# Kernel optimization log

Hardware: AMD Instinct MI355X
Metric: run time of the kernel (lower is better)

The kernel has to match this reference:

```python
import jax, jax.numpy as jnp
import numpy as np

VOCAB, D = 10000, 32
QUEUE_LEN = 100


def setup_inputs() -> dict:
    key = jax.random.key(0)
    ks = jax.random.split(key, 8)
    B, T = 64, 1024
    s = 0.1
    return dict(
        inputs=jax.random.randint(ks[0], (B, T), 0, 10000, dtype=jnp.int32),
        emb=jax.random.normal(ks[1], (VOCAB, D), dtype=jnp.float32) * s,
        k_lstm=jax.random.normal(ks[2], (D, 4 * D), dtype=jnp.float32) * s,
        rk_lstm=jax.random.normal(ks[3], (D, 4 * D), dtype=jnp.float32) * s,
        b_lstm=jnp.zeros((4 * D,), dtype=jnp.float32),
        W1=jax.random.normal(ks[4], (D, D), dtype=jnp.float32) * s,
        b1=jnp.zeros((D,), dtype=jnp.float32),
        W2=jax.random.normal(ks[5], (D, 1), dtype=jnp.float32) * s,
        b2=jnp.zeros((1,), dtype=jnp.float32),
    )


def _lstm(x, k, rk, b):
    # Keras LSTM, gate order [i, f, g(cell), o], sigmoid recurrent act, tanh act.
    B, T, D = x.shape
    xg = jnp.einsum('btd,de->bte', x, k) + b  # precompute input projections

    def step(carry, xg_t):
        h, c = carry
        z = xg_t + h @ rk
        i, f, g, o = jnp.split(z, 4, axis=-1)
        c = jax.nn.sigmoid(f) * c + jax.nn.sigmoid(i) * jnp.tanh(g)
        h = jax.nn.sigmoid(o) * jnp.tanh(c)
        return (h, c), h

    init = (jnp.zeros((B, D), x.dtype), jnp.zeros((B, D), x.dtype))
    _, hs = jax.lax.scan(step, init, jnp.swapaxes(xg, 0, 1))  # [T,B,D]
    return jnp.swapaxes(hs, 0, 1)  # [B,T,D]


def _zero_index_queue(x_ids):
    # Vectorized replacement of the (i,j) Python scan: last QUEUE_LEN positions
    # (row-major order) where token==0, as [QUEUE_LEN,2] int32, padded with -1.
    B, T = x_ids.shape
    flat = (x_ids == 0).reshape(-1)
    N = flat.shape[0]
    ridx = jnp.nonzero(flat[::-1], size=QUEUE_LEN, fill_value=-1)[0]
    pos = jnp.where(ridx >= 0, N - 1 - ridx, -1)[::-1]  # ascending, like deque
    ii = jnp.where(pos >= 0, pos // T, -1)
    jj = jnp.where(pos >= 0, pos % T, -1)
    return jnp.stack([ii, jj], axis=-1).astype(jnp.int32)


def _forward_float(x_ids, emb, k_lstm, rk_lstm, b_lstm, W1, b1, W2, b2):
    x = emb[x_ids]                                  # [B,T,D]
    h = _lstm(x, k_lstm, rk_lstm, b_lstm)           # [B,T,D]
    scores = jnp.einsum('btd,bsd->bts', h, h)       # unscaled dot attention
    attn = jax.nn.softmax(scores, axis=-1)
    ctx = jnp.einsum('bts,bsd->btd', attn, h)       # Keras Attention output
    y = jnp.einsum('btd,bte->bde', ctx, h)          # Dot(axes=(1,1)) -> [B,D,D]
    y = jax.nn.relu(y @ W1 + b1)
    return jax.nn.sigmoid(y @ W2 + b2)              # [B,D,1]


def reference(inputs, emb, k_lstm, rk_lstm, b_lstm, W1, b1, W2, b2):
    x_ids = jnp.where(inputs < VOCAB, inputs, 0)
    out = _forward_float(x_ids, emb, k_lstm, rk_lstm, b_lstm, W1, b1, W2, b2)
    return out, _zero_index_queue(x_ids)
```

## Files before the change

### kernel.cpp

```cpp
#include <hip/hip_runtime.h>
#include <math.h>

#define BB 64
#define TT 1024
#define DD 32
#define GG 128
#define VOCABN 10000
#define QLEN 100

typedef short short8 __attribute__((ext_vector_type(8)));
typedef float floatx4 __attribute__((ext_vector_type(4)));
typedef float floatx2 __attribute__((ext_vector_type(2)));
typedef unsigned short u16;

__device__ __forceinline__ float fsig(float x) {
    return __builtin_amdgcn_rcpf(1.0f + __expf(-x));
}
__device__ __forceinline__ float readlane_f(float v, int l) {
    return __int_as_float(__builtin_amdgcn_readlane(__float_as_int(v), l));
}
__device__ __forceinline__ u16 f2bf_rne(float x) {
    unsigned u = __float_as_uint(x);
    u += 0x7FFF + ((u >> 16) & 1);
    return (u16)(u >> 16);
}
__device__ __forceinline__ float bf2f(u16 s) {
    return __uint_as_float(((unsigned)s) << 16);
}
__device__ __forceinline__ floatx2 fma2(float s, floatx2 w, floatx2 acc) {
    return __builtin_elementwise_fma((floatx2){s, s}, w, acc);
}

#define UU 8
__global__
__attribute__((amdgpu_flat_work_group_size(128, 128)))
__attribute__((amdgpu_waves_per_eu(1, 1)))
void k_lstm_scan(const int* __restrict__ ids,
                 const float* __restrict__ emb,
                 const float* __restrict__ klstm,
                 const float* __restrict__ bias,
                 const float* __restrict__ rk,
                 u16* __restrict__ hh, u16* __restrict__ hl,
                 u16* __restrict__ th, u16* __restrict__ tl,
                 int* __restrict__ list,
                 float* __restrict__ outq) {
    const int b = blockIdx.x;
    const int tid = threadIdx.x;
    const int wv = tid >> 6;
    const int l = tid & 63;
    if (b >= BB) {
        if (wv != 0) return;
        const int4* v4 = (const int4*)ids;
        const int C4 = (BB * TT) / 4 / 64;
        const int b4 = l * C4;
        int cnt = 0;
#pragma unroll 4
        for (int i = 0; i < C4; ++i) {
            int4 v = v4[b4 + i];
            cnt += (v.x == 0 || (unsigned)v.x >= VOCABN);
            cnt += (v.y == 0 || (unsigned)v.y >= VOCABN);
            cnt += (v.z == 0 || (unsigned)v.z >= VOCABN);
            cnt += (v.w == 0 || (unsigned)v.w >= VOCABN);
        }
        int scan = cnt;
#pragma unroll
        for (int o = 1; o < 64; o <<= 1) {
            int nn = __shfl_up(scan, o);
            if (l >= o) scan += nn;
        }
        const int total = __shfl(scan, 63);
        int off = scan - cnt;
        const int base = l * (C4 * 4);
#pragma unroll 4
        for (int i = 0; i < C4; ++i) {
            int4 v = v4[b4 + i];
            if (v.x == 0 || (unsigned)v.x >= VOCABN) list[off++] = base + 4 * i;
            if (v.y == 0 || (unsigned)v.y >= VOCABN) list[off++] = base + 4 * i + 1;
            if (v.z == 0 || (unsigned)v.z >= VOCABN) list[off++] = base + 4 * i + 2;
            if (v.w == 0 || (unsigned)v.w >= VOCABN) list[off++] = base + 4 * i + 3;
        }
        __threadfence();
        const int Kc = total < QLEN ? total : QLEN;
        for (int t = l; t < QLEN; t += 64) {
            float ii = -1.0f, jj = -1.0f;
            if (t >= QLEN - Kc) {
                int pos = list[total - QLEN + t];
                ii = (float)(pos >> 10);
                jj = (float)(pos & (TT - 1));
            }
            outq[2 * t] = ii;
            outq[2 * t + 1] = jj;
        }
        return;
    }

    __shared__ float ring[2][UU][GG];
    __shared__ __align__(16) float hring[2][UU][DD];
    const int* idsb = ids + b * TT;

    if (wv == 1) {
        const int ja = l, jb = l + 64;
        floatx2 kp[DD];
#pragma unroll
        for (int d2 = 0; d2 < DD; ++d2)
            kp[d2] = (floatx2){klstm[d2 * GG + ja], klstm[d2 * GG + jb]};
        const floatx2 bj = (floatx2){bias[ja], bias[jb]};
        const int dd = l & 31;
        const int u_r = l >> 3, dc = (l & 7) * 4;
        const int d_c = l & 31, ug = (l >> 5) * 4;
        u16* hhb = hh + (size_t)b * TT * DD;
        u16* hlb = hl + (size_t)b * TT * DD;
        u16* thb = th + (size_t)b * DD * TT;
        u16* tlb = tl + (size_t)b * DD * TT;

#define PROD_TOKEN(SEL, U, EV)                                               \
        {                                                                    \
            floatx2 z0 = bj;                                                 \
            floatx2 z1 = {0.f, 0.f}, z2 = {0.f, 0.f}, z3 = {0.f, 0.f};       \
            _Pragma("unroll")                                                \
            for (int k = 0; k < DD; k += 4) {                                \
                float e0 = readlane_f(EV, k);                                \
                float e1 = readlane_f(EV, k + 1);                            \
                float e2 = readlane_f(EV, k + 2);                            \
                float e3 = readlane_f(EV, k + 3);                            \
                z0 = fma2(e0, kp[k], z0);                                    \
                z1 = fma2(e1, kp[k + 1], z1);                                \
                z2 = fma2(e2, kp[k + 2], z2);                                \
                z3 = fma2(e3, kp[k + 3], z3);                                \
            }                                                                \
            floatx2 zf = (z0 + z1) + (z2 + z3);                              \
            ring[SEL][U][ja] = zf.x;                                         \
            ring[SEL][U][jb] = zf.y;                                         \
        }

#define CVT_CHUNK(HSEL, TC0)                                                 \
        {                                                                    \
            const float4 hv4 = *(const float4*)&hring[HSEL][u_r][dc];        \
            float xr[4] = {hv4.x, hv4.y, hv4.z, hv4.w};                      \
            u16 rh[4], rl[4];                                                \
            _Pragma("unroll")                                                \
            for (int i = 0; i < 4; ++i) {                                    \
                rh[i] = f2bf_rne(xr[i]);                                     \
                rl[i] = f2bf_rne(xr[i] - bf2f(rh[i]));                       \
            }                                                                \
            ushort4 rhv = {rh[0], rh[1], rh[2], rh[3]};                      \
            ushort4 rlv = {rl[0], rl[1], rl[2], rl[3]};                      \
            *(ushort4*)&hhb[(size_t)((TC0) + u_r) * DD + dc] = rhv;          \
            *(ushort4*)&hlb[(size_t)((TC0) + u_r) * DD + dc] = rlv;          \
            u16 ch[4], cl[4];                                                \
            _Pragma("unroll")                                                \
            for (int j = 0; j < 4; ++j) {                                    \
                float x = hring[HSEL][ug + j][d_c];                          \
                ch[j] = f2bf_rne(x);                                         \
                cl[j] = f2bf_rne(x - bf2f(ch[j]));                           \
            }                                                                \
            ushort4 chv = {ch[0], ch[1], ch[2], ch[3]};                      \
            ushort4 clv = {cl[0], cl[1], cl[2], cl[3]};                      \
            *(ushort4*)&thb[(size_t)d_c * TT + (TC0) + ug] = chv;            \
            *(ushort4*)&tlb[(size_t)d_c * TT + (TC0) + ug] = clv;            \
        }

        {
            int id0 = idsb[0]; if ((unsigned)id0 >= VOCABN) id0 = 0;
            float ec = emb[id0 * DD + dd];
#pragma unroll
            for (int u = 0; u < UU; ++u) {
                float en = 0.f;
                if (u + 1 < UU) {
                    int idn = idsb[u + 1]; if ((unsigned)idn >= VOCABN) idn = 0;
                    en = emb[idn * DD + dd];
                }
                PROD_TOKEN(0, u, ec)
                ec = en;
            }
        }
        __syncthreads();
        int sel = 0;
        for (int t0 = 0; t0 < TT; t0 += UU) {
            if (t0 + UU < TT) {
                const int s = sel ^ 1;
                int id0 = idsb[t0 + UU]; if ((unsigned)id0 >= VOCABN) id0 = 0;
                float ec = emb[id0 * DD + dd];
#pragma unroll
                for (int u = 0; u < UU; ++u) {
                    float en = 0.f;
                    if (u + 1 < UU) {
                        int tn = t0 + UU + u + 1;
                        if (tn > TT - 1) tn = TT - 1;
                        int idn = idsb[tn]; if ((unsigned)idn >= VOCABN) idn = 0;
                        en = emb[idn * DD + dd];
                    }
                    PROD_TOKEN(s, u, ec)
                    ec = en;
                }
            }
            if (t0) CVT_CHUNK((t0 / UU - 1) & 1, t0 - UU)
            __syncthreads();
            sel ^= 1;
        }
        CVT_CHUNK(1, TT - UU)
#undef PROD_TOKEN
#undef CVT_CHUNK
        return;
    }

    const int d = l & 31;
    const bool hi = l >= 32;
    const int ga = (hi ? 32 : 0) + d;
    const int gb = (hi ? 96 : 64) + d;
    floatx2 rkp[DD];
#pragma unroll
    for (int k = 0; k < DD; ++k)
        rkp[k] = (floatx2){rk[k * GG + ga], rk[k * GG + gb]};

    float h = 0.0f, c = 0.0f;
    __syncthreads();
    int sel = 0;
    for (int t0 = 0; t0 < TT; t0 += UU) {
        float pa[UU], pb[UU];
#pragma unroll
        for (int u = 0; u < UU; ++u) {
            pa[u] = ring[sel][u][ga];
            pb[u] = ring[sel][u][gb];
        }
#pragma unroll
        for (int u = 0; u < UU; ++u) {
            floatx2 x0 = {pa[u], pb[u]};
            floatx2 x1 = {0.f, 0.f}, x2 = {0.f, 0.f}, x3 = {0.f, 0.f};
#pragma unroll
            for (int k = 0; k < DD; k += 4) {
                float h0 = readlane_f(h, k);
                float h1 = readlane_f(h, k + 1);
                float h2 = readlane_f(h, k + 2);
                float h3 = readlane_f(h, k + 3);
                x0 = fma2(h0, rkp[k],     x0);
                x1 = fma2(h1, rkp[k + 1], x1);
                x2 = fma2(h2, rkp[k + 2], x2);
                x3 = fma2(h3, rkp[k + 3], x3);
            }
            floatx2 zf = (x0 + x1) + (x2 + x3);
            float za = zf.x, zb = zf.y;
            float a = fsig(za);
            float zbm = hi ? zb : 2.0f * zb;
            float s2 = fsig(zbm);
            float bv = hi ? s2 : 2.0f * s2 - 1.0f;
            auto r1 = __builtin_amdgcn_permlane32_swap(
                __float_as_int(bv), __float_as_int(a), false, false);
            auto r2 = __builtin_amdgcn_permlane32_swap(
                __float_as_int(a), __float_as_int(bv), false, false);
            float fg = __int_as_float(r1[0]);
            float og = __int_as_float(r2[0]);
            c = fmaf(fg, c, a * bv);
            float tc = 2.0f * fsig(2.0f * c) - 1.0f;
            h = og * tc;
            if (!hi) hring[sel][u][d] = h;
        }
        __syncthreads();
        sel ^= 1;
    }
}

__global__ __launch_bounds__(512, 1) void k_attn(const u16* __restrict__ hh,
                                                 const u16* __restrict__ hl,
                                                 const u16* __restrict__ th,
                                                 const u16* __restrict__ tl,
                                                 u16* __restrict__ cth,
                                                 u16* __restrict__ ctl) {
    __shared__ __align__(16) char smem[88064];
    const int tid = threadIdx.x;
    const int w = tid >> 6;
    const int wt = w & 3;
    const int kh = w >> 2;
    const int l = tid & 63;
    const int m = l & 15;
    const int g = l >> 4;
    const int b = blockIdx.x & 63;
    const int qt = (blockIdx.x >> 6) * 4 + wt;
    const int q0 = qt * 64;
    const int e0 = kh * 512;
    const size_t rb = (size_t)b * TT * DD;
    const size_t tb = (size_t)b * DD * TT;
    u16* plw = (u16*)(smem + w * 10240);

    const short8 Qh0 = *(const short8*)&hh[rb + (size_t)(q0 + m) * DD + g * 8];
    const short8 Ql0 = *(const short8*)&hl[rb + (size_t)(q0 + m) * DD + g * 8];
    const short8 Qh1 = *(const short8*)&hh[rb + (size_t)(q0 + 16 + m) * DD + g * 8];
    const short8 Ql1 = *(const short8*)&hl[rb + (size_t)(q0 + 16 + m) * DD + g * 8];
    const short8 Qh2 = *(const short8*)&hh[rb + (size_t)(q0 + 32 + m) * DD + g * 8];
    const short8 Ql2 = *(const short8*)&hl[rb + (size_t)(q0 + 32 + m) * DD + g * 8];
    const short8 Qh3 = *(const short8*)&hh[rb + (size_t)(q0 + 48 + m) * DD + g * 8];
    const short8 Ql3 = *(const short8*)&hl[rb + (size_t)(q0 + 48 + m) * DD + g * 8];
    short8 ONES;
#pragma unroll
    for (int j = 0; j < 8; ++j) ONES[j] = (short)0x3F80;

    floatx4 c0 = {0.f, 0.f, 0.f, 0.f}, c1 = {0.f, 0.f, 0.f, 0.f};
    floatx4 c2 = {0.f, 0.f, 0.f, 0.f}, c3 = {0.f, 0.f, 0.f, 0.f};
    floatx4 c4 = {0.f, 0.f, 0.f, 0.f}, c5 = {0.f, 0.f, 0.f, 0.f};
    floatx4 c6 = {0.f, 0.f, 0.f, 0.f}, c7 = {0.f, 0.f, 0.f, 0.f};
    floatx4 la0 = {0.f, 0.f, 0.f, 0.f}, la1 = {0.f, 0.f, 0.f, 0.f};
    floatx4 la2 = {0.f, 0.f, 0.f, 0.f}, la3 = {0.f, 0.f, 0.f, 0.f};

#define S_BLOCK(QH, QL, KH_A, KL_A, KH_B, KL_B, SA, SB)                       \
    SA = __builtin_amdgcn_mfma_f32_16x16x32_bf16(QH, KH_A, SA, 0, 0, 0);      \
    SA = __builtin_amdgcn_mfma_f32_16x16x32_bf16(QH, KL_A, SA, 0, 0, 0);      \
    SA = __builtin_amdgcn_mfma_f32_16x16x32_bf16(QL, KH_A, SA, 0, 0, 0);      \
    SB = __builtin_amdgcn_mfma_f32_16x16x32_bf16(QH, KH_B, SB, 0, 0, 0);      \
    SB = __builtin_amdgcn_mfma_f32_16x16x32_bf16(QH, KL_B, SB, 0, 0, 0);      \
    SB = __builtin_amdgcn_mfma_f32_16x16x32_bf16(QL, KH_B, SB, 0, 0, 0);

#define EXP_STORE(SA, SB, TILE, SLOT)                                         \
    {                                                                         \
        u16* lp = plw + ((TILE) * 2 + (SLOT)) * 640;                          \
        _Pragma("unroll")                                                     \
        for (int r = 0; r < 4; ++r) {                                         \
            lp[(g * 4 + r) * 40 + m]      = f2bf_rne(__expf(SA[r]));          \
            lp[(g * 4 + r) * 40 + 16 + m] = f2bf_rne(__expf(SB[r]));          \
        }                                                                     \
    }

#define SPANEL(KhA, KlA, KhB, KlB, SLOT)                                      \
    {                                                                         \
        floatx4 sA = {0.f, 0.f, 0.f, 0.f}, sB = {0.f, 0.f, 0.f, 0.f};         \
        floatx4 tA = {0.f, 0.f, 0.f, 0.f}, tB = {0.f, 0.f, 0.f, 0.f};         \
        floatx4 uA = {0.f, 0.f, 0.f, 0.f}, uB = {0.f, 0.f, 0.f, 0.f};         \
        floatx4 vA = {0.f, 0.f, 0.f, 0.f}, vB = {0.f, 0.f, 0.f, 0.f};         \
        S_BLOCK(Qh0, Ql0, KhA, KlA, KhB, KlB, sA, sB)                         \
        S_BLOCK(Qh1, Ql1, KhA, KlA, KhB, KlB, tA, tB)                         \
        S_BLOCK(Qh2, Ql2, KhA, KlA, KhB, KlB, uA, uB)                         \
        S_BLOCK(Qh3, Ql3, KhA, KlA, KhB, KlB, vA, vB)                         \
        EXP_STORE(sA, sB, 0, SLOT)                                            \
        EXP_STORE(tA, tB, 1, SLOT)                                            \
        EXP_STORE(uA, uB, 2, SLOT)                                            \
        EXP_STORE(vA, vB, 3, SLOT)                                            \
    }

#define PV_TILE(T, CA, CB, LAc, SLOTP, VH0, VL0, VH1, VL1)                    \
    {                                                                         \
        const short8 P = *(const short8*)&plw[((T) * 2 + (SLOTP)) * 640 + m * 40 + g * 8]; \
        CA  = __builtin_amdgcn_mfma_f32_16x16x32_bf16(P, VH0, CA, 0, 0, 0);   \
        CA  = __builtin_amdgcn_mfma_f32_16x16x32_bf16(P, VL0, CA, 0, 0, 0);   \
        CB  = __builtin_amdgcn_mfma_f32_16x16x32_bf16(P, VH1, CB, 0, 0, 0);   \
        CB  = __builtin_amdgcn_mfma_f32_16x16x32_bf16(P, VL1, CB, 0, 0, 0);   \
        LAc = __builtin_amdgcn_mfma_f32_16x16x32_bf16(P, ONES, LAc, 0, 0, 0); \
    }

#define PV_PANEL(SLOTP, VH0, VL0, VH1, VL1)                                   \
    PV_TILE(0, c0, c1, la0, SLOTP, VH0, VL0, VH1, VL1)                        \
    PV_TILE(1, c2, c3, la1, SLOTP, VH0, VL0, VH1, VL1)                        \
    PV_TILE(2, c4, c5, la2, SLOTP, VH0, VL0, VH1, VL1)                        \
    PV_TILE(3, c6, c7, la3, SLOTP, VH0, VL0, VH1, VL1)

#define LOAD_K(BASE, RA, RLA, RB, RLB)                                        \
    RA  = *(const short8*)&hh[rb + (size_t)((BASE) + m) * DD + g * 8];        \
    RLA = *(const short8*)&hl[rb + (size_t)((BASE) + m) * DD + g * 8];        \
    RB  = *(const short8*)&hh[rb + (size_t)((BASE) + 16 + m) * DD + g * 8];   \
    RLB = *(const short8*)&hl[rb + (size_t)((BASE) + 16 + m) * DD + g * 8];

#define LOAD_V(BASE, RH0, RL0, RH1, RL1)                                      \
    RH0 = *(const short8*)&th[tb + (size_t)m * TT + (BASE) + g * 8];          \
    RL0 = *(const short8*)&tl[tb + (size_t)m * TT + (BASE) + g * 8];          \
    RH1 = *(const short8*)&th[tb + (size_t)(16 + m) * TT + (BASE) + g * 8];   \
    RL1 = *(const short8*)&tl[tb + (size_t)(16 + m) * TT + (BASE) + g * 8];

    {
        short8 KA, KLA, KB, KLB;
        LOAD_K(e0, KA, KLA, KB, KLB)
        SPANEL(KA, KLA, KB, KLB, 0)
    }
    short8 Vh0, Vl0, Vh1, Vl1, KhA, KlA, KhB, KlB;
    LOAD_V(e0, Vh0, Vl0, Vh1, Vl1)
    LOAD_K(e0 + 32, KhA, KlA, KhB, KlB)

#pragma unroll 1
    for (int j = 1; j < 16; ++j) {
        const int knK = (j < 15) ? e0 + 32 * (j + 1) : 0;
        const int knV = e0 + 32 * j;
        short8 nKhA, nKlA, nKhB, nKlB, nVh0, nVl0, nVh1, nVl1;
        LOAD_K(knK, nKhA, nKlA, nKhB, nKlB)
        LOAD_V(knV, nVh0, nVl0, nVh1, nVl1)

        SPANEL(KhA, KlA, KhB, KlB, j & 1)
        PV_PANEL((j - 1) & 1, Vh0, Vl0, Vh1, Vl1)

        KhA = nKhA; KlA = nKlA; KhB = nKhB; KlB = nKlB;
        Vh0 = nVh0; Vl0 = nVl0; Vh1 = nVh1; Vl1 = nVl1;
    }
    PV_PANEL(1, Vh0, Vl0, Vh1, Vl1)
#undef S_BLOCK
#undef EXP_STORE
#undef SPANEL
#undef PV_TILE
#undef PV_PANEL
#undef LOAD_K
#undef LOAD_V

    __syncthreads();
    if (w >= 4) {
        floatx4* dst = (floatx4*)(smem + wt * 13312 + l * 208);
        dst[0] = c0;  dst[1] = c1;  dst[2] = c2;  dst[3] = c3;
        dst[4] = c4;  dst[5] = c5;  dst[6] = c6;  dst[7] = c7;
        dst[8] = la0; dst[9] = la1; dst[10] = la2; dst[11] = la3;
    }
    __syncthreads();
    if (w >= 4) return;
    {
        const floatx4* src = (const floatx4*)(smem + wt * 13312 + l * 208);
        c0 += src[0];  c1 += src[1];  c2 += src[2];  c3 += src[3];
        c4 += src[4];  c5 += src[5];  c6 += src[6];  c7 += src[7];
        la0 += src[8]; la1 += src[9]; la2 += src[10]; la3 += src[11];
    }

    float (*ct)[34] = (float (*)[34])(smem + 53248 + w * 8704);
#pragma unroll
    for (int r = 0; r < 4; ++r) {
        float li0 = __builtin_amdgcn_rcpf(la0[r]);
        float li1 = __builtin_amdgcn_rcpf(la1[r]);
        float li2 = __builtin_amdgcn_rcpf(la2[r]);
        float li3 = __builtin_amdgcn_rcpf(la3[r]);
        ct[g * 4 + r][m]            = c0[r] * li0;
        ct[g * 4 + r][16 + m]       = c1[r] * li0;
        ct[16 + g * 4 + r][m]       = c2[r] * li1;
        ct[16 + g * 4 + r][16 + m]  = c3[r] * li1;
        ct[32 + g * 4 + r][m]       = c4[r] * li2;
        ct[32 + g * 4 + r][16 + m]  = c5[r] * li2;
        ct[48 + g * 4 + r][m]       = c6[r] * li3;
        ct[48 + g * 4 + r][16 + m]  = c7[r] * li3;
    }
    const int srow = l >> 3;
    const int tcol = (l & 7) * 8;
#pragma unroll
    for (int cblk = 0; cblk < 4; ++cblk) {
        const int dr = cblk * 8 + srow;
        short8 hvec, lvec;
#pragma unroll
        for (int j2 = 0; j2 < 8; ++j2) {
            float v = ct[tcol + j2][dr];
            u16 hv = f2bf_rne(v);
            hvec[j2] = (short)hv;
            lvec[j2] = (short)f2bf_rne(v - bf2f(hv));
        }
        *(short8*)&cth[tb + (size_t)dr * TT + q0 + tcol] = hvec;
        *(short8*)&ctl[tb + (size_t)dr * TT + q0 + tcol] = lvec;
    }
}

__global__ __launch_bounds__(256) void k_ymlp(const u16* __restrict__ cth,
                                              const u16* __restrict__ ctl,
                                              const u16* __restrict__ th,
                                              const u16* __restrict__ tl,
                                              const float* __restrict__ W1,
                                              const float* __restrict__ b1,
                                              const float* __restrict__ W2,
                                              const float* __restrict__ b2,
                                              float* __restrict__ out) {
    const int b = blockIdx.x;
    const int tid = threadIdx.x;
    const int w = tid >> 6;
    const int l = tid & 63;
    const int m = l & 15;
    const int g = l >> 4;
    const size_t tb = (size_t)b * DD * TT;
    const int k0 = w * (TT / 4);

    floatx4 y00 = {0.f, 0.f, 0.f, 0.f}, y01 = {0.f, 0.f, 0.f, 0.f};
    floatx4 y10 = {0.f, 0.f, 0.f, 0.f}, y11 = {0.f, 0.f, 0.f, 0.f};
#pragma unroll 2
    for (int ks = 0; ks < TT / 4; ks += 32) {
        const size_t kk = (size_t)(k0 + ks + g * 8);
        short8 A0h = *(const short8*)&cth[tb + (size_t)m * TT + kk];
        short8 A0l = *(const short8*)&ctl[tb + (size_t)m * TT + kk];
        short8 A1h = *(const short8*)&cth[tb + (size_t)(16 + m) * TT + kk];
        short8 A1l = *(const short8*)&ctl[tb + (size_t)(16 + m) * TT + kk];
        short8 B0h = *(const short8*)&th[tb + (size_t)m * TT + kk];
        short8 B0l = *(const short8*)&tl[tb + (size_t)m * TT + kk];
        short8 B1h = *(const short8*)&th[tb + (size_t)(16 + m) * TT + kk];
        short8 B1l = *(const short8*)&tl[tb + (size_t)(16 + m) * TT + kk];
        y00 = __builtin_amdgcn_mfma_f32_16x16x32_bf16(A0h, B0h, y00, 0, 0, 0);
        y00 = __builtin_amdgcn_mfma_f32_16x16x32_bf16(A0h, B0l, y00, 0, 0, 0);
        y00 = __builtin_amdgcn_mfma_f32_16x16x32_bf16(A0l, B0h, y00, 0, 0, 0);
        y01 = __builtin_amdgcn_mfma_f32_16x16x32_bf16(A0h, B1h, y01, 0, 0, 0);
        y01 = __builtin_amdgcn_mfma_f32_16x16x32_bf16(A0h, B1l, y01, 0, 0, 0);
        y01 = __builtin_amdgcn_mfma_f32_16x16x32_bf16(A0l, B1h, y01, 0, 0, 0);
        y10 = __builtin_amdgcn_mfma_f32_16x16x32_bf16(A1h, B0h, y10, 0, 0, 0);
        y10 = __builtin_amdgcn_mfma_f32_16x16x32_bf16(A1h, B0l, y10, 0, 0, 0);
        y10 = __builtin_amdgcn_mfma_f32_16x16x32_bf16(A1l, B0h, y10, 0, 0, 0);
        y11 = __builtin_amdgcn_mfma_f32_16x16x32_bf16(A1h, B1h, y11, 0, 0, 0);
        y11 = __builtin_amdgcn_mfma_f32_16x16x32_bf16(A1h, B1l, y11, 0, 0, 0);
        y11 = __builtin_amdgcn_mfma_f32_16x16x32_bf16(A1l, B1h, y11, 0, 0, 0);
    }
    __shared__ float ysp[4][DD][DD];
#pragma unroll
    for (int r = 0; r < 4; ++r) {
        ysp[w][g * 4 + r][m]           = y00[r];
        ysp[w][g * 4 + r][16 + m]      = y01[r];
        ysp[w][16 + g * 4 + r][m]      = y10[r];
        ysp[w][16 + g * 4 + r][16 + m] = y11[r];
    }
    __syncthreads();
    const int e = tid & 31;
    const int d4 = (tid >> 5) * 4;
    __shared__ float ys[DD][DD];
#pragma unroll
    for (int r = 0; r < 4; ++r)
        ys[d4 + r][e] = (ysp[0][d4 + r][e] + ysp[1][d4 + r][e])
                      + (ysp[2][d4 + r][e] + ysp[3][d4 + r][e]);
    __syncthreads();
    __shared__ float yr[DD][33];
#pragma unroll
    for (int r = 0; r < 4; ++r) {
        float v = b1[e];
#pragma unroll
        for (int ee = 0; ee < DD; ++ee) v += ys[d4 + r][ee] * W1[ee * DD + e];
        yr[d4 + r][e] = fmaxf(v, 0.0f);
    }
    __syncthreads();
    if (tid < DD) {
        float v = b2[0];
#pragma unroll
        for (int ee = 0; ee < DD; ++ee) v += yr[tid][ee] * W2[ee];
        out[b * DD + tid] = 1.0f / (1.0f + expf(-v));
    }
}

extern "C" void kernel_launch(void* const* d_in, const int* in_sizes, int n_in,
                              void* d_out, int out_size, void* d_ws, size_t ws_size,
                              hipStream_t stream) {
    const int* ids   = (const int*)d_in[0];
    const float* emb = (const float*)d_in[1];
    const float* kl  = (const float*)d_in[2];
    const float* rk  = (const float*)d_in[3];
    const float* bl  = (const float*)d_in[4];
    const float* W1  = (const float*)d_in[5];
    const float* b1  = (const float*)d_in[6];
    const float* W2  = (const float*)d_in[7];
    const float* b2  = (const float*)d_in[8];
    float* out = (float*)d_out;

    char* ws = (char*)d_ws;
    const size_t H_ELEMS = (size_t)BB * TT * DD;
    u16* hh   = (u16*)ws;
    u16* hl   = (u16*)(ws + H_ELEMS * 2);
    u16* th   = (u16*)(ws + H_ELEMS * 4);
    u16* tl   = (u16*)(ws + H_ELEMS * 6);
    u16* cth  = (u16*)(ws + H_ELEMS * 8 + H_ELEMS * 4);
    u16* ctl  = (u16*)(ws + H_ELEMS * 8 + H_ELEMS * 4 + H_ELEMS * 2);
    int* list = (int*)(ws + H_ELEMS * 8 + H_ELEMS * 8);

    k_lstm_scan<<<BB + 1, 128, 0, stream>>>(ids, emb, kl, bl, rk,
                                            hh, hl, th, tl, list, out + BB * DD);
    k_attn<<<BB * 4, 512, 0, stream>>>(hh, hl, th, tl, cth, ctl);
    k_ymlp<<<BB, 256, 0, stream>>>(cth, ctl, th, tl, W1, b1, W2, b2, out);
}
```

Before: 348.5 us.

## Fuse ctx·h outer-product into attention kernel, emit per-tile partial Y

The attention kernel now splits its normalized context tile into bf16 hi/lo pairs in registers and multiplies it directly against the transposed h tile with MFMA. Each 64-query tile writes a 32x32 partial Y to a workspace buffer. The later kernel only sums the 16 partials per batch and runs the MLP. This removes the global write and re-read of the full ctx tensor in hi/lo form and shrinks the final kernel's work, at the cost of extra MFMA work and register pressure at the end of the attention kernel.

```diff
diff --git a/kernel.cpp b/kernel.cpp
--- a/kernel.cpp
+++ b/kernel.cpp
@@ -264,8 +264,7 @@
                                                  const u16* __restrict__ hl,
                                                  const u16* __restrict__ th,
                                                  const u16* __restrict__ tl,
-                                                 u16* __restrict__ cth,
-                                                 u16* __restrict__ ctl) {
+                                                 float* __restrict__ ypart) {
     __shared__ __align__(16) char smem[88064];
     const int tid = threadIdx.x;
     const int w = tid >> 6;
@@ -393,7 +392,6 @@
 #undef PV_TILE
 #undef PV_PANEL
 #undef LOAD_K
-#undef LOAD_V
 
     __syncthreads();
     if (w >= 4) {
@@ -427,55 +425,26 @@
         ct[48 + g * 4 + r][m]       = c6[r] * li3;
         ct[48 + g * 4 + r][16 + m]  = c7[r] * li3;
     }
-    const int srow = l >> 3;
-    const int tcol = (l & 7) * 8;
-#pragma unroll
-    for (int cblk = 0; cblk < 4; ++cblk) {
-        const int dr = cblk * 8 + srow;
-        short8 hvec, lvec;
-#pragma unroll
-        for (int j2 = 0; j2 < 8; ++j2) {
-            float v = ct[tcol + j2][dr];
-            u16 hv = f2bf_rne(v);
-            hvec[j2] = (short)hv;
-            lvec[j2] = (short)f2bf_rne(v - bf2f(hv));
-        }
-        *(short8*)&cth[tb + (size_t)dr * TT + q0 + tcol] = hvec;
-        *(short8*)&ctl[tb + (size_t)dr * TT + q0 + tcol] = lvec;
-    }
-}
-
-__global__ __launch_bounds__(256) void k_ymlp(const u16* __restrict__ cth,
-                                              const u16* __restrict__ ctl,
-                                              const u16* __restrict__ th,
-                                              const u16* __restrict__ tl,
-                                              const float* __restrict__ W1,
-                                              const float* __restrict__ b1,
-                                              const float* __restrict__ W2,
-                                              const float* __restrict__ b2,
-                                              float* __restrict__ out) {
-    const int b = blockIdx.x;
-    const int tid = threadIdx.x;
-    const int w = tid >> 6;
-    const int l = tid & 63;
-    const int m = l & 15;
-    const int g = l >> 4;
-    const size_t tb = (size_t)b * DD * TT;
-    const int k0 = w * (TT / 4);
 
     floatx4 y00 = {0.f, 0.f, 0.f, 0.f}, y01 = {0.f, 0.f, 0.f, 0.f};
     floatx4 y10 = {0.f, 0.f, 0.f, 0.f}, y11 = {0.f, 0.f, 0.f, 0.f};
-#pragma unroll 2
-    for (int ks = 0; ks < TT / 4; ks += 32) {
-        const size_t kk = (size_t)(k0 + ks + g * 8);
-        short8 A0h = *(const short8*)&cth[tb + (size_t)m * TT + kk];
-        short8 A0l = *(const short8*)&ctl[tb + (size_t)m * TT + kk];
-        short8 A1h = *(const short8*)&cth[tb + (size_t)(16 + m) * TT + kk];
-        short8 A1l = *(const short8*)&ctl[tb + (size_t)(16 + m) * TT + kk];
-        short8 B0h = *(const short8*)&th[tb + (size_t)m * TT + kk];
-        short8 B0l = *(const short8*)&tl[tb + (size_t)m * TT + kk];
-        short8 B1h = *(const short8*)&th[tb + (size_t)(16 + m) * TT + kk];
-        short8 B1l = *(const short8*)&tl[tb + (size_t)(16 + m) * TT + kk];
+#pragma unroll
+    for (int ch = 0; ch < 2; ++ch) {
+        const int tloc = ch * 32 + g * 8;
+        short8 A0h, A0l, A1h, A1l;
+#pragma unroll
+        for (int j = 0; j < 8; ++j) {
+            float v0 = ct[tloc + j][m];
+            u16 h0 = f2bf_rne(v0);
+            A0h[j] = (short)h0;
+            A0l[j] = (short)f2bf_rne(v0 - bf2f(h0));
+            float v1 = ct[tloc + j][16 + m];
+            u16 h1 = f2bf_rne(v1);
+            A1h[j] = (short)h1;
+            A1l[j] = (short)f2bf_rne(v1 - bf2f(h1));
+        }
+        short8 B0h, B0l, B1h, B1l;
+        LOAD_V(q0 + ch * 32, B0h, B0l, B1h, B1l)
         y00 = __builtin_amdgcn_mfma_f32_16x16x32_bf16(A0h, B0h, y00, 0, 0, 0);
         y00 = __builtin_amdgcn_mfma_f32_16x16x32_bf16(A0h, B0l, y00, 0, 0, 0);
         y00 = __builtin_amdgcn_mfma_f32_16x16x32_bf16(A0l, B0h, y00, 0, 0, 0);
@@ -489,22 +458,37 @@
         y11 = __builtin_amdgcn_mfma_f32_16x16x32_bf16(A1h, B1l, y11, 0, 0, 0);
         y11 = __builtin_amdgcn_mfma_f32_16x16x32_bf16(A1l, B1h, y11, 0, 0, 0);
     }
-    __shared__ float ysp[4][DD][DD];
+#undef LOAD_V
+    float* yp = ypart + ((size_t)b * 16 + qt) * (DD * DD);
 #pragma unroll
     for (int r = 0; r < 4; ++r) {
-        ysp[w][g * 4 + r][m]           = y00[r];
-        ysp[w][g * 4 + r][16 + m]      = y01[r];
-        ysp[w][16 + g * 4 + r][m]      = y10[r];
-        ysp[w][16 + g * 4 + r][16 + m] = y11[r];
-    }
-    __syncthreads();
+        yp[(g * 4 + r) * DD + m]            = y00[r];
+        yp[(g * 4 + r) * DD + 16 + m]       = y01[r];
+        yp[(16 + g * 4 + r) * DD + m]       = y10[r];
+        yp[(16 + g * 4 + r) * DD + 16 + m]  = y11[r];
+    }
+}
+
+__global__ __launch_bounds__(256) void k_tail(const float* __restrict__ ypart,
+                                              const float* __restrict__ W1,
+                                              const float* __restrict__ b1,
+                                              const float* __restrict__ W2,
+                                              const float* __restrict__ b2,
+                                              float* __restrict__ out) {
+    const int b = blockIdx.x;
+    const int tid = threadIdx.x;
     const int e = tid & 31;
     const int d4 = (tid >> 5) * 4;
+    const float* yb = ypart + (size_t)b * 16 * (DD * DD);
     __shared__ float ys[DD][DD];
 #pragma unroll
-    for (int r = 0; r < 4; ++r)
-        ys[d4 + r][e] = (ysp[0][d4 + r][e] + ysp[1][d4 + r][e])
-                      + (ysp[2][d4 + r][e] + ysp[3][d4 + r][e]);
+    for (int r = 0; r < 4; ++r) {
+        float s = 0.f;
+#pragma unroll
+        for (int p = 0; p < 16; ++p)
+            s += yb[p * (DD * DD) + (d4 + r) * DD + e];
+        ys[d4 + r][e] = s;
+    }
     __syncthreads();
     __shared__ float yr[DD][33];
 #pragma unroll
@@ -543,12 +527,11 @@
     u16* hl   = (u16*)(ws + H_ELEMS * 2);
     u16* th   = (u16*)(ws + H_ELEMS * 4);
     u16* tl   = (u16*)(ws + H_ELEMS * 6);
-    u16* cth  = (u16*)(ws + H_ELEMS * 8 + H_ELEMS * 4);
-    u16* ctl  = (u16*)(ws + H_ELEMS * 8 + H_ELEMS * 4 + H_ELEMS * 2);
+    float* ypart = (float*)(ws + H_ELEMS * 8);
     int* list = (int*)(ws + H_ELEMS * 8 + H_ELEMS * 8);
 
     k_lstm_scan<<<BB + 1, 128, 0, stream>>>(ids, emb, kl, bl, rk,
                                             hh, hl, th, tl, list, out + BB * DD);
-    k_attn<<<BB * 4, 512, 0, stream>>>(hh, hl, th, tl, cth, ctl);
-    k_ymlp<<<BB, 256, 0, stream>>>(cth, ctl, th, tl, W1, b1, W2, b2, out);
-}
+    k_attn<<<BB * 4, 512, 0, stream>>>(hh, hl, th, tl, ypart);
+    k_tail<<<BB, 256, 0, stream>>>(ypart, W1, b1, W2, b2, out);
+}
```

Result: no change. 342.0 us (median of 2 runs) (-1.9%).
